# Kernel tuning notes

Measured on AMD Instinct MI355X. Metric: run time of the kernel, lower is better.

The kernel has to match this reference:

```python
import jax, jax.numpy as jnp
import numpy as np


def _slopes(y, x):
    # Finite-difference slopes along the last axis, extended to length N:
    # one-sided at endpoints, averaged in the interior (standard Hermite tangents).
    m = (y[..., 1:] - y[..., :-1]) / (x[1:] - x[:-1])  # [..., N-1]
    return jnp.concatenate(
        [m[..., :1], 0.5 * (m[..., 1:] + m[..., :-1]), m[..., -1:]], axis=-1
    )  # [..., N]


def _interp1d(y, x0, m, xs):
    # y, m: [..., N]; x0: [N] sorted; xs: [Q] queries -> [..., Q]
    I = jnp.searchsorted(x0[1:-1], xs)          # bucket index in [0, N-2]
    x_lo = x0[I]
    dx = x0[I + 1] - x_lo
    t = (xs - x_lo) / dx
    t2 = t * t
    t3 = t2 * t
    h00 = 1.0 - 3.0 * t2 + 2.0 * t3   # A row 0: [1,0,-3,2]
    h10 = t - 2.0 * t2 + t3           # A row 1: [0,1,-2,1]
    h01 = 3.0 * t2 - 2.0 * t3         # A row 2: [0,0,3,-2]
    h11 = t3 - t2                     # A row 3: [0,0,-1,1]
    y_lo = jnp.take(y, I, axis=-1)
    y_hi = jnp.take(y, I + 1, axis=-1)
    m_lo = jnp.take(m, I, axis=-1)
    m_hi = jnp.take(m, I + 1, axis=-1)
    return h00 * y_lo + h10 * m_lo * dx + h01 * y_hi + h11 * m_hi * dx


def setup_inputs() -> dict:
    key = jax.random.key(0)
    k_sig, k_xs, k_ys = jax.random.split(key, 3)
    B, H, W = 32, 512, 512
    Nx, Ny = 1024, 1024
    signal = jax.random.normal(k_sig, (B, H, W), dtype=jnp.float32)
    x1 = jnp.arange(W, dtype=jnp.float32)  # sorted axis for last dim
    x2 = jnp.arange(H, dtype=jnp.float32)  # sorted axis for second-to-last dim
    xs = jnp.sort(jax.random.uniform(k_xs, (Nx,), dtype=jnp.float32) * (W - 1))
    ys = jnp.sort(jax.random.uniform(k_ys, (Ny,), dtype=jnp.float32) * (H - 1))
    return {"signal": signal, "x1": x1, "x2": x2, "xs": xs, "ys": ys}


def reference(signal, x1, x2, xs, ys):
    # Pass 1: interpolate along W at xs -> [B, H, Nx]
    m1 = _slopes(signal, x1)
    out = _interp1d(signal, x1, m1, xs)
    # Pass 2: interpolate along H at ys (operate on transposed data) -> [B, Nx, Ny]
    out_t = jnp.swapaxes(out, -1, -2)   # [B, Nx, H]
    m2 = _slopes(out_t, x2)
    out2 = _interp1d(out_t, x2, m2, ys)
    return jnp.swapaxes(out2, -1, -2)   # [B, Ny, Nx]
```

## Files before the change

### kernel.cpp

```cpp
#include <hip/hip_runtime.h>

#define B_  32
#define H_  512
#define W_  512
#define NX_ 1024
#define NY_ 1024
#define R_  8
#define NB  (H_ / R_)
#define STG (R_ + 3)
#define MAXQ 64

#define SROW    576
#define SLOTS_R 144
#define NSLOT   (STG * SLOTS_R)

__device__ __forceinline__ float4 f4mul(float s, float4 a) {
    return make_float4(s * a.x, s * a.y, s * a.z, s * a.w);
}
__device__ __forceinline__ float4 f4fma(float s, float4 a, float4 acc) {
    acc.x += s * a.x; acc.y += s * a.y; acc.z += s * a.z; acc.w += s * a.w;
    return acc;
}

__device__ __forceinline__ void gload_lds16(const float* g, float* l) {
    __builtin_amdgcn_global_load_lds(
        (const __attribute__((address_space(1))) void*)g,
        (__attribute__((address_space(3))) void*)l,
        16, 0, 0);
}

__device__ __forceinline__ void hermite_window(float x, int N, int& c0, float4& v) {
    int i = (int)floorf(x);
    i = min(max(i, 0), N - 2);
    float t  = x - (float)i;
    float t2 = t * t;
    float t3 = t2 * t;
    float h00 = 1.0f - 3.0f * t2 + 2.0f * t3;
    float h10 = t - 2.0f * t2 + t3;
    float h01 = 3.0f * t2 - 2.0f * t3;
    float h11 = t3 - t2;
    if (i == 0) {
        c0 = 0;
        v = make_float4(h00 - h10 - 0.5f * h11, h01 + h10, 0.5f * h11, 0.0f);
    } else if (i == N - 2) {
        c0 = i - 1;
        v = make_float4(-0.5f * h10, h00 - h11, h01 + 0.5f * h10 + h11, 0.0f);
    } else {
        c0 = i - 1;
        v = make_float4(-0.5f * h10, h00 - 0.5f * h11, h01 + 0.5f * h10, 0.5f * h11);
    }
}

__global__ __launch_bounds__(256) void fused(
    const float* __restrict__ sig,
    const float* __restrict__ xs,
    const float* __restrict__ ys,
    float* __restrict__ out)
{
    __shared__ float stage[NSLOT * 4];
    __shared__ float4 wy_s[MAXQ];
    __shared__ int   slot_s[MAXQ];
    __shared__ int   parts[4];

    const int tid  = threadIdx.x;
    const int band = blockIdx.x;
    const int b    = blockIdx.y;
    const int r0   = band * R_;

    const float* sb = sig + (size_t)b * H_ * W_;
    float* stf = stage;
    #pragma unroll
    for (int it = 0; it < 6; ++it) {
        int j   = it * 256 + tid;
        int s   = j / SLOTS_R;
        int k   = j - s * SLOTS_R;
        int g   = k / 9;
        int sub = k - g * 9;
        int gr  = min(max(r0 - 1 + s, 0), H_ - 1);
        int idx = min(8 * g + sub, 127);
        gload_lds16(sb + (size_t)gr * W_ + idx * 4, stf + (size_t)j * 4);
    }
    if (tid < NSLOT - 1536) {
        int j   = 1536 + tid;
        int s   = j / SLOTS_R;
        int k   = j - s * SLOTS_R;
        int g   = k / 9;
        int sub = k - g * 9;
        int gr  = min(max(r0 - 1 + s, 0), H_ - 1);
        int idx = min(8 * g + sub, 127);
        *(float4*)(stf + (size_t)j * 4) = ((const float4*)(sb + (size_t)gr * W_))[idx];
    }

    const int qxb = tid * 4;
    const float4 xq = *(const float4*)(xs + qxb);
    int c0a, c0b, c0c, c0d;
    float4 w0, w1, w2, w3;
    hermite_window(xq.x, W_, c0a, w0);
    hermite_window(xq.y, W_, c0b, w1);
    hermite_window(xq.z, W_, c0c, w2);
    hermite_window(xq.w, W_, c0d, w3);
    const int b0 = c0a + ((c0a >> 5) << 2);
    const int b1 = c0b + ((c0b >> 5) << 2);
    const int b2 = c0c + ((c0c >> 5) << 2);
    const int b3 = c0d + ((c0d >> 5) << 2);

    {
        const float r0f = (float)r0;
        const float r1f = (float)(r0 + R_);
        const float4 y4 = *(const float4*)(ys + tid * 4);
        int clo = (y4.x < r0f) + (y4.y < r0f) + (y4.z < r0f) + (y4.w < r0f);
        int chi = (y4.x < r1f) + (y4.y < r1f) + (y4.z < r1f) + (y4.w < r1f);
        int pk = clo | (chi << 16);
        #pragma unroll
        for (int d = 32; d; d >>= 1) pk += __shfl_down(pk, d);
        if ((tid & 63) == 0) parts[tid >> 6] = pk;
    }
    __syncthreads();

    const int tot = parts[0] + parts[1] + parts[2] + parts[3];
    const int qyA = tot & 0xFFFF;
    const int nq  = (tot >> 16) - qyA;

    float4 c[STG];
    #pragma unroll
    for (int s = 0; s < STG; ++s) {
        const float* sr = stf + s * SROW;
        c[s].x = w0.x * sr[b0] + w0.y * sr[b0 + 1] + w0.z * sr[b0 + 2] + w0.w * sr[b0 + 3];
        c[s].y = w1.x * sr[b1] + w1.y * sr[b1 + 1] + w1.z * sr[b1 + 2] + w1.w * sr[b1 + 3];
        c[s].z = w2.x * sr[b2] + w2.y * sr[b2 + 1] + w2.z * sr[b2 + 2] + w2.w * sr[b2 + 3];
        c[s].w = w3.x * sr[b3] + w3.y * sr[b3 + 1] + w3.z * sr[b3 + 2] + w3.w * sr[b3 + 3];
    }

    if (tid < nq && tid < MAXQ) {
        int ry; float4 wv;
        hermite_window(ys[qyA + tid], H_, ry, wv);
        wy_s[tid]   = wv;
        slot_s[tid] = ry - r0 + 1;
    }
    __syncthreads();

    float* op = out + (size_t)b * NY_ * NX_ + (size_t)qyA * NX_ + qxb;
    for (int j = 0; j < nq; ++j, op += NX_) {
        float4 wv; int s0;
        if (j < MAXQ) { wv = wy_s[j]; s0 = slot_s[j]; }
        else {
            int ry; hermite_window(ys[qyA + j], H_, ry, wv); s0 = ry - r0 + 1;
        }
        s0 = __builtin_amdgcn_readfirstlane(s0);
        float4 acc;
        #define CASE_(S) case S: \
            acc = f4fma(wv.w, c[S + 3], f4fma(wv.z, c[S + 2], \
                  f4fma(wv.y, c[S + 1], f4mul(wv.x, c[S])))); break;
        switch (s0) {
            CASE_(0) CASE_(1) CASE_(2) CASE_(3)
            CASE_(4) CASE_(5) CASE_(6) CASE_(7)
            default: acc = make_float4(0.f, 0.f, 0.f, 0.f); break;
        }
        #undef CASE_
        *(float4*)op = acc;
    }
}

extern "C" void kernel_launch(void* const* d_in, const int* in_sizes, int n_in,
                              void* d_out, int out_size, void* d_ws, size_t ws_size,
                              hipStream_t stream) {
    const float* signal = (const float*)d_in[0];
    const float* xs = (const float*)d_in[3];
    const float* ys = (const float*)d_in[4];
    float* out = (float*)d_out;

    dim3 grid(NB, B_);
    fused<<<grid, 256, 0, stream>>>(signal, xs, ys, out);
}
```

Baseline: 177.8 us.

## Process four row bands per block with double-buffered async LDS staging

Each block now handles four consecutive 8-row bands instead of one, so the grid shrinks from 64 to 16 blocks per batch. The next band's rows are prefetched into a second LDS buffer with global_load_lds while the current band is computed and written. Row staging changes to 16-float4 groups padded to 17 slots, which adds fewer padding slots per row. Per-band y-query counts are packed into 64-bit prefix sums. The aim is to hide global load latency and amortize setup; the cost is fewer blocks and less parallelism, plus more LDS use per block.

```diff
diff --git a/kernel.cpp b/kernel.cpp
--- a/kernel.cpp
+++ b/kernel.cpp
@@ -6,13 +6,16 @@
 #define NX_ 1024
 #define NY_ 1024
 #define R_  8
-#define NB  (H_ / R_)
-#define STG (R_ + 3)
-#define MAXQ 64
-
-#define SROW    576
-#define SLOTS_R 144
-#define NSLOT   (STG * SLOTS_R)
+#define NB  64
+#define STG 11
+#define NT_ 4
+#define NGB (NB / NT_)
+#define GQ_ 128
+
+#define SLOT_G  17
+#define SLOTS_R 136
+#define SROW    544
+#define NSB     1536
 
 __device__ __forceinline__ float4 f4mul(float s, float4 a) {
     return make_float4(s * a.x, s * a.y, s * a.z, s * a.w);
@@ -51,45 +54,39 @@
     }
 }
 
+__device__ __forceinline__ void issue_band(const float* sb, int r0, float* buf, int tid) {
+    #pragma unroll
+    for (int it = 0; it < 6; ++it) {
+        int j   = it * 256 + tid;
+        int s   = min(j / SLOTS_R, STG - 1);
+        int k   = j - s * SLOTS_R;
+        int g   = k / SLOT_G;
+        int sub = k - g * SLOT_G;
+        int gr  = min(max(r0 - 1 + s, 0), H_ - 1);
+        int idx = min(16 * g + sub, 127);
+        gload_lds16(sb + (size_t)gr * W_ + idx * 4, buf + (size_t)j * 4);
+    }
+}
+
 __global__ __launch_bounds__(256) void fused(
     const float* __restrict__ sig,
     const float* __restrict__ xs,
     const float* __restrict__ ys,
     float* __restrict__ out)
 {
-    __shared__ float stage[NSLOT * 4];
-    __shared__ float4 wy_s[MAXQ];
-    __shared__ int   slot_s[MAXQ];
-    __shared__ int   parts[4];
-
-    const int tid  = threadIdx.x;
-    const int band = blockIdx.x;
-    const int b    = blockIdx.y;
-    const int r0   = band * R_;
+    __shared__ float bufs[2][NSB * 4];
+    __shared__ float4 wy_s[GQ_];
+    __shared__ int    slotA_s[GQ_];
+    __shared__ unsigned long long partsU[4];
+
+    const int tid = threadIdx.x;
+    const int bg  = blockIdx.x;
+    const int b   = blockIdx.y;
+    const int rb0 = bg * NT_ * R_;
 
     const float* sb = sig + (size_t)b * H_ * W_;
-    float* stf = stage;
-    #pragma unroll
-    for (int it = 0; it < 6; ++it) {
-        int j   = it * 256 + tid;
-        int s   = j / SLOTS_R;
-        int k   = j - s * SLOTS_R;
-        int g   = k / 9;
-        int sub = k - g * 9;
-        int gr  = min(max(r0 - 1 + s, 0), H_ - 1);
-        int idx = min(8 * g + sub, 127);
-        gload_lds16(sb + (size_t)gr * W_ + idx * 4, stf + (size_t)j * 4);
-    }
-    if (tid < NSLOT - 1536) {
-        int j   = 1536 + tid;
-        int s   = j / SLOTS_R;
-        int k   = j - s * SLOTS_R;
-        int g   = k / 9;
-        int sub = k - g * 9;
-        int gr  = min(max(r0 - 1 + s, 0), H_ - 1);
-        int idx = min(8 * g + sub, 127);
-        *(float4*)(stf + (size_t)j * 4) = ((const float4*)(sb + (size_t)gr * W_))[idx];
-    }
+
+    issue_band(sb, rb0, &bufs[0][0], tid);
 
     const int qxb = tid * 4;
     const float4 xq = *(const float4*)(xs + qxb);
@@ -99,65 +96,94 @@
     hermite_window(xq.y, W_, c0b, w1);
     hermite_window(xq.z, W_, c0c, w2);
     hermite_window(xq.w, W_, c0d, w3);
-    const int b0 = c0a + ((c0a >> 5) << 2);
-    const int b1 = c0b + ((c0b >> 5) << 2);
-    const int b2 = c0c + ((c0c >> 5) << 2);
-    const int b3 = c0d + ((c0d >> 5) << 2);
+    const int b0 = c0a + ((c0a >> 6) << 2);
+    const int b1 = c0b + ((c0b >> 6) << 2);
+    const int b2 = c0c + ((c0c >> 6) << 2);
+    const int b3 = c0d + ((c0d >> 6) << 2);
 
     {
-        const float r0f = (float)r0;
-        const float r1f = (float)(r0 + R_);
+        unsigned long long pk = 0;
         const float4 y4 = *(const float4*)(ys + tid * 4);
-        int clo = (y4.x < r0f) + (y4.y < r0f) + (y4.z < r0f) + (y4.w < r0f);
-        int chi = (y4.x < r1f) + (y4.y < r1f) + (y4.z < r1f) + (y4.w < r1f);
-        int pk = clo | (chi << 16);
+        #pragma unroll
+        for (int k = 0; k < 5; ++k) {
+            float bnd = (float)(rb0 + R_ * k);
+            int cc = (y4.x < bnd) + (y4.y < bnd) + (y4.z < bnd) + (y4.w < bnd);
+            pk += (unsigned long long)cc << (12 * k);
+        }
         #pragma unroll
         for (int d = 32; d; d >>= 1) pk += __shfl_down(pk, d);
-        if ((tid & 63) == 0) parts[tid >> 6] = pk;
+        if ((tid & 63) == 0) partsU[tid >> 6] = pk;
     }
     __syncthreads();
 
-    const int tot = parts[0] + parts[1] + parts[2] + parts[3];
-    const int qyA = tot & 0xFFFF;
-    const int nq  = (tot >> 16) - qyA;
-
-    float4 c[STG];
+    const unsigned long long cnt = partsU[0] + partsU[1] + partsU[2] + partsU[3];
+    const int qyA0 = (int)(cnt & 0xFFF);
+    const int nqg  = (int)((cnt >> 48) & 0xFFF) - qyA0;
+
+    if (tid < nqg && tid < GQ_) {
+        int ry; float4 wv;
+        hermite_window(ys[qyA0 + tid], H_, ry, wv);
+        wy_s[tid]    = wv;
+        slotA_s[tid] = ry;
+    }
+
     #pragma unroll
-    for (int s = 0; s < STG; ++s) {
-        const float* sr = stf + s * SROW;
-        c[s].x = w0.x * sr[b0] + w0.y * sr[b0 + 1] + w0.z * sr[b0 + 2] + w0.w * sr[b0 + 3];
-        c[s].y = w1.x * sr[b1] + w1.y * sr[b1 + 1] + w1.z * sr[b1 + 2] + w1.w * sr[b1 + 3];
-        c[s].z = w2.x * sr[b2] + w2.y * sr[b2 + 1] + w2.z * sr[b2 + 2] + w2.w * sr[b2 + 3];
-        c[s].w = w3.x * sr[b3] + w3.y * sr[b3 + 1] + w3.z * sr[b3 + 2] + w3.w * sr[b3 + 3];
-    }
-
-    if (tid < nq && tid < MAXQ) {
-        int ry; float4 wv;
-        hermite_window(ys[qyA + tid], H_, ry, wv);
-        wy_s[tid]   = wv;
-        slot_s[tid] = ry - r0 + 1;
-    }
-    __syncthreads();
-
-    float* op = out + (size_t)b * NY_ * NX_ + (size_t)qyA * NX_ + qxb;
-    for (int j = 0; j < nq; ++j, op += NX_) {
-        float4 wv; int s0;
-        if (j < MAXQ) { wv = wy_s[j]; s0 = slot_s[j]; }
-        else {
-            int ry; hermite_window(ys[qyA + j], H_, ry, wv); s0 = ry - r0 + 1;
-        }
-        s0 = __builtin_amdgcn_readfirstlane(s0);
-        float4 acc;
-        #define CASE_(S) case S: \
-            acc = f4fma(wv.w, c[S + 3], f4fma(wv.z, c[S + 2], \
-                  f4fma(wv.y, c[S + 1], f4mul(wv.x, c[S])))); break;
-        switch (s0) {
-            CASE_(0) CASE_(1) CASE_(2) CASE_(3)
-            CASE_(4) CASE_(5) CASE_(6) CASE_(7)
-            default: acc = make_float4(0.f, 0.f, 0.f, 0.f); break;
-        }
-        #undef CASE_
-        *(float4*)op = acc;
+    for (int t = 0; t < NT_; ++t) {
+        const int r0 = rb0 + t * R_;
+        const float* bufc = &bufs[t & 1][0];
+
+        if (t + 1 < NT_)
+            issue_band(sb, r0 + R_, &bufs[(t + 1) & 1][0], tid);
+
+        if (t > 0) {
+            if (t + 1 < NT_) {
+                asm volatile("s_waitcnt vmcnt(6) lgkmcnt(0)" ::: "memory");
+            } else {
+                asm volatile("s_waitcnt vmcnt(0) lgkmcnt(0)" ::: "memory");
+            }
+            __builtin_amdgcn_sched_barrier(0);
+            __builtin_amdgcn_s_barrier();
+        }
+
+        float4 c[STG];
+        #pragma unroll
+        for (int s = 0; s < STG; ++s) {
+            const float* sr = bufc + s * SROW;
+            c[s].x = w0.x * sr[b0] + w0.y * sr[b0 + 1] + w0.z * sr[b0 + 2] + w0.w * sr[b0 + 3];
+            c[s].y = w1.x * sr[b1] + w1.y * sr[b1 + 1] + w1.z * sr[b1 + 2] + w1.w * sr[b1 + 3];
+            c[s].z = w2.x * sr[b2] + w2.y * sr[b2 + 1] + w2.z * sr[b2 + 2] + w2.w * sr[b2 + 3];
+            c[s].w = w3.x * sr[b3] + w3.y * sr[b3 + 1] + w3.z * sr[b3 + 2] + w3.w * sr[b3 + 3];
+        }
+
+        const int qyA   = (int)((cnt >> (12 * t)) & 0xFFF);
+        const int nq    = (int)((cnt >> (12 * (t + 1))) & 0xFFF) - qyA;
+        const int gbase = qyA - qyA0;
+
+        asm volatile("s_waitcnt lgkmcnt(0)" ::: "memory");
+        __builtin_amdgcn_sched_barrier(0);
+        __builtin_amdgcn_s_barrier();
+
+        float* op = out + (size_t)b * NY_ * NX_ + (size_t)qyA * NX_ + qxb;
+        for (int j = 0; j < nq; ++j, op += NX_) {
+            const int gi = gbase + j;
+            float4 wv; int sA;
+            if (gi < GQ_) { wv = wy_s[gi]; sA = slotA_s[gi]; }
+            else {
+                int ry; hermite_window(ys[qyA + j], H_, ry, wv); sA = ry;
+            }
+            const int s0 = __builtin_amdgcn_readfirstlane(sA) - r0 + 1;
+            float4 acc;
+            #define CASE_(S) case S: \
+                acc = f4fma(wv.w, c[S + 3], f4fma(wv.z, c[S + 2], \
+                      f4fma(wv.y, c[S + 1], f4mul(wv.x, c[S])))); break;
+            switch (s0) {
+                CASE_(0) CASE_(1) CASE_(2) CASE_(3)
+                CASE_(4) CASE_(5) CASE_(6) CASE_(7)
+                default: acc = make_float4(0.f, 0.f, 0.f, 0.f); break;
+            }
+            #undef CASE_
+            *(float4*)op = acc;
+        }
     }
 }
 
@@ -169,6 +195,6 @@
     const float* ys = (const float*)d_in[4];
     float* out = (float*)d_out;
 
-    dim3 grid(NB, B_);
+    dim3 grid(NGB, B_);
     fused<<<grid, 256, 0, stream>>>(signal, xs, ys, out);
 }
```

Measured after the change: 177.3 us. Within noise of the previous version (-0.3%).
